# Kernel optimization log

Hardware: AMD Instinct MI355X
Metric: run time of the kernel (lower is better)

## Reference

```python
import jax, jax.numpy as jnp
import numpy as np

NBINS_PIX = 256   # uint8 pixel values
NBINS_MEAN = 512  # neighbor mean fits in [0, 408] for side=1


def setup_inputs() -> dict:
    key = jax.random.key(0)
    # uniform [0,1) so x.max() < 1.0 branch (x*255 quantization) is taken, as in the source
    x = jax.random.uniform(key, (64, 1024, 1024), dtype=jnp.float32)
    return {"x": x}


def reference(x):
    H, W = x.shape[-2:]
    x = jax.lax.stop_gradient(x)  # mirrors .clone().detach()
    xf = x.reshape(-1, H, W)
    B = xf.shape[0]
    # quantize: (x*255).to(uint8) if max<1 else x.to(uint8); uint8 cast truncates
    scale = jnp.where(jnp.max(xf) < 1.0, jnp.float32(255.0), jnp.float32(1.0))
    xq = (xf * scale).astype(jnp.uint8).astype(jnp.float32)
    xi = xq.astype(jnp.int32)

    # zero-padded 8-neighbor sum (3x3 window minus center), side=1
    xp = jnp.pad(xi, ((0, 0), (1, 1), (1, 1)))
    nb = jnp.zeros_like(xi)
    for dh in range(3):
        for dw in range(3):
            if dh == 1 and dw == 1:
                continue
            nb = nb + xp[:, dh:dh + H, dw:dw + W]

    # Faithful replication of the source's normalization: the original indexes
    # mean_nb[a, b] where dim0 is the BATCH dim and dim1 is the row dim, so the
    # divisor depends on (batch, row) and broadcasts over columns.
    # t=0: num=3 at 4 (batch,row) corners; then num->5 for edges and interior.
    D = jnp.ones((B, H), dtype=jnp.float32)
    D = D.at[0, 0].set(3.0).at[-1, 0].set(3.0).at[0, -1].set(3.0).at[-1, -1].set(3.0)
    D = D.at[1:-1, 0].set(5.0).at[1:-1, -1].set(5.0)
    D = D.at[0, 1:-1].set(5.0).at[-1, 1:-1].set(5.0)
    D = D.at[1:-1, 1:-1].set(5.0)
    mean_nb = nb.astype(jnp.float32) / D[:, :, None]
    mean_i = mean_nb.astype(jnp.int32)  # trunc toward zero, values >= 0

    # joint (pixel, mean) histogram per image -> entropy, matches unique+counts
    codes = xi * NBINS_MEAN + mean_i  # in [0, 256*512)

    def hist_entropy(c):
        counts = jnp.zeros(NBINS_PIX * NBINS_MEAN, jnp.float32).at[c.reshape(-1)].add(1.0)
        p = counts / (H * W)
        safe = jnp.where(p > 0, p, 1.0)
        return jnp.sum(jnp.where(p > 0, -p * jnp.log2(safe), 0.0))

    ent = jax.vmap(hist_entropy)(codes)  # [B]
    return jnp.mean(ent)
```

## Files before the change

### kernel.cpp

```cpp
#include <hip/hip_runtime.h>

#define IMG_H 1024
#define IMG_W 1024
#define NPIX  (IMG_H * IMG_W)
#define NBINS (256 * 512)
#define TILE  64
#define LW    (TILE + 2)

#define MEANS  428
#define HBINS  (256 * MEANS)
#define HWORDS (HBINS / 4)
#define HVECS  (HWORDS / 4)
#define QUADS  4
#define QROWS  (IMG_H / QUADS)
#define TCOLS  8
#define TROWS  (QROWS / 8)

__global__ __launch_bounds__(1024) void fused_hist_kernel(const float* __restrict__ x,
                                                          unsigned int* __restrict__ partials,
                                                          int B) {
    __shared__ __align__(16) unsigned int h[HWORDS];

    const int blk  = blockIdx.x;
    const int b    = blk >> 2;
    const int quad = blk & 3;
    const int tid  = threadIdx.x;

    const float* img = x + (size_t)b * NPIX;
    const int c0    = (tid & 127) * TCOLS;
    const int strip = tid >> 7;
    const int rs    = quad * QROWS + strip * TROWS;
    const int re    = rs + TROWS;
    const bool bEdge = (b == 0) || (b == B - 1);

    auto loadraw = [&](int r, float4& f0, float4& f1, float& fl, float& fr) {
        if ((unsigned)r < IMG_H) {
            const float* row = img + r * IMG_W;
            f0 = *(const float4*)(row + c0);
            f1 = *(const float4*)(row + c0 + 4);
            fl = (c0 > 0) ? row[c0 - 1] : 0.0f;
            fr = (c0 + TCOLS < IMG_W) ? row[c0 + TCOLS] : 0.0f;
        } else {
            f0 = make_float4(0.f, 0.f, 0.f, 0.f);
            f1 = make_float4(0.f, 0.f, 0.f, 0.f);
            fl = 0.f; fr = 0.f;
        }
    };

    auto hsump = [&](const float4& f0, const float4& f1, float fl, float fr,
                     unsigned hs[4], unsigned qc[4]) {
        unsigned q0 = (unsigned)(int)(fl   * 255.0f);
        unsigned q1 = (unsigned)(int)(f0.x * 255.0f);
        unsigned q2 = (unsigned)(int)(f0.y * 255.0f);
        unsigned q3 = (unsigned)(int)(f0.z * 255.0f);
        unsigned q4 = (unsigned)(int)(f0.w * 255.0f);
        unsigned q5 = (unsigned)(int)(f1.x * 255.0f);
        unsigned q6 = (unsigned)(int)(f1.y * 255.0f);
        unsigned q7 = (unsigned)(int)(f1.z * 255.0f);
        unsigned q8 = (unsigned)(int)(f1.w * 255.0f);
        unsigned q9 = (unsigned)(int)(fr   * 255.0f);
        unsigned p0 = q0 | (q1 << 16);
        unsigned p1 = q2 | (q3 << 16);
        unsigned p2 = q4 | (q5 << 16);
        unsigned p3 = q6 | (q7 << 16);
        unsigned p4 = q8 | (q9 << 16);
        unsigned m0 = (p0 >> 16) | (p1 << 16);
        unsigned m1 = (p1 >> 16) | (p2 << 16);
        unsigned m2 = (p2 >> 16) | (p3 << 16);
        unsigned m3 = (p3 >> 16) | (p4 << 16);
        hs[0] = p0 + m0 + p1;  qc[0] = m0;
        hs[1] = p1 + m1 + p2;  qc[1] = m1;
        hs[2] = p2 + m2 + p3;  qc[2] = m2;
        hs[3] = p3 + m3 + p4;  qc[3] = m3;
    };

    unsigned hA[4], hB[4], qB[4];

    auto emit = [&](const unsigned hU[4], const unsigned hM[4], const unsigned qM[4],
                    const unsigned hL[4], bool div3) {
#pragma unroll
        for (int j = 0; j < 4; ++j) {
            unsigned nb = hU[j] + hM[j] + hL[j] - qM[j];
            unsigned n0 = nb & 0xFFFFu, n1 = nb >> 16;
            unsigned cv0 = qM[j] & 0xFFFFu, cv1 = qM[j] >> 16;
            unsigned me0 = div3 ? n0 / 3u : n0 / 5u;
            unsigned me1 = div3 ? n1 / 3u : n1 / 5u;
            unsigned bin0 = cv0 * MEANS + me0;
            unsigned bin1 = cv1 * MEANS + me1;
            atomicAdd(&h[bin0 >> 2], 1u << ((bin0 & 3u) * 8u));
            atomicAdd(&h[bin1 >> 2], 1u << ((bin1 & 3u) * 8u));
        }
    };

    auto body = [&](int r, float4& a0, float4& a1, float& al, float& ar,
                          float4& b0, float4& b1, float& bl, float& br) {
        unsigned hC[4], qC[4], hD[4], qD[4];
        hsump(a0, a1, al, ar, hC, qC);
        hsump(b0, b1, bl, br, hD, qD);
        if (r + 5 <= re) loadraw(r + 5, a0, a1, al, ar);
        if (r + 6 <= re) loadraw(r + 6, b0, b1, bl, br);
        const bool c0n = bEdge && (r == 0);
        const bool c1n = bEdge && (r + 1 == IMG_H - 1);
        emit(hA, hB, qB, hC, c0n);
        emit(hB, hC, qC, hD, c1n);
#pragma unroll
        for (int j = 0; j < 4; ++j) { hA[j] = hC[j]; hB[j] = hD[j]; qB[j] = qD[j]; }
    };

    float4 e0a, e0b, e1a, e1b;  float e0l, e0r, e1l, e1r;
    float4 n0a, n0b, n1a, n1b, n2a, n2b, n3a, n3b;
    float  n0l, n0r, n1l, n1r, n2l, n2r, n3l, n3r;
    loadraw(rs - 1, e0a, e0b, e0l, e0r);
    loadraw(rs,     e1a, e1b, e1l, e1r);
    loadraw(rs + 1, n0a, n0b, n0l, n0r);
    loadraw(rs + 2, n1a, n1b, n1l, n1r);
    loadraw(rs + 3, n2a, n2b, n2l, n2r);
    loadraw(rs + 4, n3a, n3b, n3l, n3r);

    {
        uint4* h4 = (uint4*)h;
#pragma unroll
        for (int i = 0; i < 7; ++i) {
            int idx = tid + i * 1024;
            if (idx < HVECS) h4[idx] = make_uint4(0u, 0u, 0u, 0u);
        }
    }
    __syncthreads();

    { unsigned tq[4]; hsump(e0a, e0b, e0l, e0r, hA, tq); }
    hsump(e1a, e1b, e1l, e1r, hB, qB);

    for (int r = rs; r < re; r += 4) {
        body(r,     n0a, n0b, n0l, n0r, n1a, n1b, n1l, n1r);
        body(r + 2, n2a, n2b, n2l, n2r, n3a, n3b, n3l, n3r);
    }
    __syncthreads();

    uint4* dst4 = (uint4*)(partials + (size_t)blk * HWORDS);
    const uint4* s4 = (const uint4*)h;
    for (int i = tid; i < HVECS; i += 1024) dst4[i] = s4[i];
}

__global__ __launch_bounds__(256) void merge_entropy_kernel(const unsigned int* __restrict__ partials,
                                                            double* __restrict__ acc,
                                                            int B) {
    const int w   = blockIdx.x * 256 + threadIdx.x;
    const int img = blockIdx.y;
    const unsigned int* p = partials + (size_t)img * QUADS * HWORDS + w;
    unsigned w0 = p[0], w1 = p[HWORDS], w2 = p[2 * HWORDS], w3 = p[3 * HWORDS];

    double local = 0.0;
#pragma unroll
    for (int sh = 0; sh < 32; sh += 8) {
        unsigned c = ((w0 >> sh) & 255u) + ((w1 >> sh) & 255u)
                   + ((w2 >> sh) & 255u) + ((w3 >> sh) & 255u);
        if (c) local += (double)c * (20.0 - (double)log2f((float)c));
    }
    for (int off = 32; off > 0; off >>= 1)
        local += __shfl_down(local, off, 64);

    __shared__ double sacc[4];
    const int lane = threadIdx.x & 63;
    const int wid  = threadIdx.x >> 6;
    if (lane == 0) sacc[wid] = local;
    __syncthreads();
    if (threadIdx.x == 0)
        atomicAdd(acc, sacc[0] + sacc[1] + sacc[2] + sacc[3]);
}

__global__ void finalize_kernel(const double* __restrict__ acc,
                                float* __restrict__ out, int B) {
    out[0] = (float)(acc[0] / ((double)NPIX * (double)B));
}

__global__ __launch_bounds__(256) void hist_kernel(const float* __restrict__ x,
                                                   unsigned int* __restrict__ hist,
                                                   int B) {
    __shared__ int s[LW * LW];
    const int tilesPerRow = IMG_W / TILE;
    const int tilesPerImg = (IMG_H / TILE) * tilesPerRow;
    const int b   = blockIdx.x / tilesPerImg;
    const int t   = blockIdx.x % tilesPerImg;
    const int ty0 = (t / tilesPerRow) * TILE;
    const int tx0 = (t % tilesPerRow) * TILE;
    const float* img = x + (size_t)b * NPIX;
    const int tid = threadIdx.x;

    for (int i = tid; i < LW * LW; i += 256) {
        int r = i / LW, c = i - r * LW;
        int gy = ty0 + r - 1, gx = tx0 + c - 1;
        int v = 0;
        if ((unsigned)gy < IMG_H && (unsigned)gx < IMG_W)
            v = (int)(img[gy * IMG_W + gx] * 255.0f);
        s[i] = v;
    }
    __syncthreads();

    unsigned int* hb = hist + (size_t)b * NBINS;
    const bool bEdge = (b == 0) || (b == B - 1);
    const int tx = tid & 63, sy = tid >> 6;
    const int c = tx + 1, r0 = sy * 16;

    int h0, h1, m1;
    { int a = s[r0 * LW + c - 1], m = s[r0 * LW + c], d = s[r0 * LW + c + 1]; h0 = a + m + d; }
    { int a = s[(r0 + 1) * LW + c - 1], m = s[(r0 + 1) * LW + c], d = s[(r0 + 1) * LW + c + 1]; h1 = a + m + d; m1 = m; }

    for (int ry = r0; ry < r0 + 16; ++ry) {
        int a = s[(ry + 2) * LW + c - 1], m = s[(ry + 2) * LW + c], d = s[(ry + 2) * LW + c + 1];
        int h2 = a + m + d;
        int nb = h0 + h1 + h2 - m1;
        int gy = ty0 + ry;
        unsigned mean = (unsigned)nb / 5u;
        if (bEdge && (gy == 0 || gy == IMG_H - 1)) mean = (unsigned)nb / 3u;
        atomicAdd(&hb[m1 * 512 + (int)mean], 1u);
        h0 = h1; h1 = h2; m1 = m;
    }
}

__global__ __launch_bounds__(256) void entropy_kernel(const unsigned int* __restrict__ hist,
                                                      double* __restrict__ acc, int n) {
    double local = 0.0;
    const int stride = gridDim.x * 256;
    for (int i = blockIdx.x * 256 + threadIdx.x; i < n; i += stride) {
        unsigned int cv = hist[i];
        if (cv) local += (double)cv * (20.0 - (double)log2f((float)cv));
    }
    for (int off = 32; off > 0; off >>= 1)
        local += __shfl_down(local, off, 64);
    __shared__ double sacc[4];
    const int lane = threadIdx.x & 63, wid = threadIdx.x >> 6;
    if (lane == 0) sacc[wid] = local;
    __syncthreads();
    if (threadIdx.x == 0)
        atomicAdd(acc, sacc[0] + sacc[1] + sacc[2] + sacc[3]);
}

extern "C" void kernel_launch(void* const* d_in, const int* in_sizes, int n_in,
                              void* d_out, int out_size, void* d_ws, size_t ws_size,
                              hipStream_t stream) {
    const float* x = (const float*)d_in[0];
    const int B = in_sizes[0] / NPIX;

    const size_t partBytes = (size_t)B * QUADS * HWORDS * sizeof(unsigned int);

    if (ws_size >= partBytes + 64) {
        unsigned int* partials = (unsigned int*)d_ws;
        double* acc = (double*)((char*)d_ws + partBytes);
        hipMemsetAsync(acc, 0, sizeof(double), stream);

        fused_hist_kernel<<<B * QUADS, 1024, 0, stream>>>(x, partials, B);
        merge_entropy_kernel<<<dim3(HWORDS / 256, B), 256, 0, stream>>>(partials, acc, B);
        finalize_kernel<<<1, 1, 0, stream>>>(acc, (float*)d_out, B);
    } else {
        unsigned int* hist = (unsigned int*)d_ws;
        const size_t histBytes = (size_t)B * NBINS * sizeof(unsigned int);
        double* acc = (double*)((char*)d_ws + histBytes);
        hipMemsetAsync(d_ws, 0, histBytes + sizeof(double), stream);

        const int tilesPerImg = (IMG_H / TILE) * (IMG_W / TILE);
        hist_kernel<<<B * tilesPerImg, 256, 0, stream>>>(x, hist, B);
        entropy_kernel<<<1024, 256, 0, stream>>>(hist, acc, B * NBINS);
        finalize_kernel<<<1, 1, 0, stream>>>(acc, (float*)d_out, B);
    }
}
```

Measured before the change: 455.5 us.

## Split histogram atomics between shared-memory and global per-image histograms

Half of the pixel rows now emit their histogram increments as global-memory atomics into a per-image 512-stride histogram, while the other half still use the packed 8-bit shared-memory histogram. The intent is to relieve contention on LDS atomics by spreading the traffic across two memory paths, and possibly to ease the 8-bit counter load. The cost is a zero-fill of a large global buffer (64 images x 128K bins x 4 bytes), slower global atomics, and an extra read of that buffer in the merge kernel, which maps each merged word back to its global bins.

```diff
diff --git a/kernel.cpp b/kernel.cpp
--- a/kernel.cpp
+++ b/kernel.cpp
@@ -18,6 +18,7 @@
 
 __global__ __launch_bounds__(1024) void fused_hist_kernel(const float* __restrict__ x,
                                                           unsigned int* __restrict__ partials,
+                                                          unsigned int* __restrict__ ghist,
                                                           int B) {
     __shared__ __align__(16) unsigned int h[HWORDS];
 
@@ -27,6 +28,7 @@
     const int tid  = threadIdx.x;
 
     const float* img = x + (size_t)b * NPIX;
+    unsigned int* gh = ghist + (size_t)b * NBINS;
     const int c0    = (tid & 127) * TCOLS;
     const int strip = tid >> 7;
     const int rs    = quad * QROWS + strip * TROWS;
@@ -76,8 +78,8 @@
 
     unsigned hA[4], hB[4], qB[4];
 
-    auto emit = [&](const unsigned hU[4], const unsigned hM[4], const unsigned qM[4],
-                    const unsigned hL[4], bool div3) {
+    auto emitL = [&](const unsigned hU[4], const unsigned hM[4], const unsigned qM[4],
+                     const unsigned hL[4], bool div3) {
 #pragma unroll
         for (int j = 0; j < 4; ++j) {
             unsigned nb = hU[j] + hM[j] + hL[j] - qM[j];
@@ -91,6 +93,19 @@
             atomicAdd(&h[bin1 >> 2], 1u << ((bin1 & 3u) * 8u));
         }
     };
+    auto emitG = [&](const unsigned hU[4], const unsigned hM[4], const unsigned qM[4],
+                     const unsigned hL[4], bool div3) {
+#pragma unroll
+        for (int j = 0; j < 4; ++j) {
+            unsigned nb = hU[j] + hM[j] + hL[j] - qM[j];
+            unsigned n0 = nb & 0xFFFFu, n1 = nb >> 16;
+            unsigned cv0 = qM[j] & 0xFFFFu, cv1 = qM[j] >> 16;
+            unsigned me0 = div3 ? n0 / 3u : n0 / 5u;
+            unsigned me1 = div3 ? n1 / 3u : n1 / 5u;
+            atomicAdd(&gh[(cv0 << 9) + me0], 1u);
+            atomicAdd(&gh[(cv1 << 9) + me1], 1u);
+        }
+    };
 
     auto body = [&](int r, float4& a0, float4& a1, float& al, float& ar,
                           float4& b0, float4& b1, float& bl, float& br) {
@@ -101,8 +116,8 @@
         if (r + 6 <= re) loadraw(r + 6, b0, b1, bl, br);
         const bool c0n = bEdge && (r == 0);
         const bool c1n = bEdge && (r + 1 == IMG_H - 1);
-        emit(hA, hB, qB, hC, c0n);
-        emit(hB, hC, qC, hD, c1n);
+        emitL(hA, hB, qB, hC, c0n);
+        emitG(hB, hC, qC, hD, c1n);
 #pragma unroll
         for (int j = 0; j < 4; ++j) { hA[j] = hC[j]; hB[j] = hD[j]; qB[j] = qD[j]; }
     };
@@ -141,7 +156,14 @@
     for (int i = tid; i < HVECS; i += 1024) dst4[i] = s4[i];
 }
 
+__global__ __launch_bounds__(256) void zero_kernel(uint4* __restrict__ p, int n4) {
+    int i = blockIdx.x * 256 + threadIdx.x;
+    const int stride = gridDim.x * 256;
+    for (; i < n4; i += stride) p[i] = make_uint4(0u, 0u, 0u, 0u);
+}
+
 __global__ __launch_bounds__(256) void merge_entropy_kernel(const unsigned int* __restrict__ partials,
+                                                            const unsigned int* __restrict__ ghist,
                                                             double* __restrict__ acc,
                                                             int B) {
     const int w   = blockIdx.x * 256 + threadIdx.x;
@@ -149,11 +171,17 @@
     const unsigned int* p = partials + (size_t)img * QUADS * HWORDS + w;
     unsigned w0 = p[0], w1 = p[HWORDS], w2 = p[2 * HWORDS], w3 = p[3 * HWORDS];
 
+    const int q  = w / (MEANS / 4);
+    const int m4 = (w - q * (MEANS / 4)) * 4;
+    const uint4 gv = *(const uint4*)(ghist + (size_t)img * NBINS + (q << 9) + m4);
+    const unsigned gvv[4] = {gv.x, gv.y, gv.z, gv.w};
+
     double local = 0.0;
 #pragma unroll
     for (int sh = 0; sh < 32; sh += 8) {
         unsigned c = ((w0 >> sh) & 255u) + ((w1 >> sh) & 255u)
-                   + ((w2 >> sh) & 255u) + ((w3 >> sh) & 255u);
+                   + ((w2 >> sh) & 255u) + ((w3 >> sh) & 255u)
+                   + gvv[sh >> 3];
         if (c) local += (double)c * (20.0 - (double)log2f((float)c));
     }
     for (int off = 32; off > 0; off >>= 1)
@@ -241,15 +269,18 @@
     const float* x = (const float*)d_in[0];
     const int B = in_sizes[0] / NPIX;
 
-    const size_t partBytes = (size_t)B * QUADS * HWORDS * sizeof(unsigned int);
-
-    if (ws_size >= partBytes + 64) {
+    const size_t partBytes  = (size_t)B * QUADS * HWORDS * sizeof(unsigned int);
+    const size_t ghistBytes = (size_t)B * NBINS * sizeof(unsigned int);
+
+    if (ws_size >= partBytes + ghistBytes + 64) {
         unsigned int* partials = (unsigned int*)d_ws;
-        double* acc = (double*)((char*)d_ws + partBytes);
+        unsigned int* ghist    = (unsigned int*)((char*)d_ws + partBytes);
+        double* acc = (double*)((char*)d_ws + partBytes + ghistBytes);
         hipMemsetAsync(acc, 0, sizeof(double), stream);
 
-        fused_hist_kernel<<<B * QUADS, 1024, 0, stream>>>(x, partials, B);
-        merge_entropy_kernel<<<dim3(HWORDS / 256, B), 256, 0, stream>>>(partials, acc, B);
+        zero_kernel<<<2048, 256, 0, stream>>>((uint4*)ghist, B * NBINS / 4);
+        fused_hist_kernel<<<B * QUADS, 1024, 0, stream>>>(x, partials, ghist, B);
+        merge_entropy_kernel<<<dim3(HWORDS / 256, B), 256, 0, stream>>>(partials, ghist, acc, B);
         finalize_kernel<<<1, 1, 0, stream>>>(acc, (float*)d_out, B);
     } else {
         unsigned int* hist = (unsigned int*)d_ws;
```

Result: slower. 1.614 ms (+254.2%).
